# Performance work log

Measured on AMD Instinct MI355X. Metric: run time of the kernel, lower is better.

The kernel has to match this reference:

```python
import jax, jax.numpy as jnp
import numpy as np

B, H, W = 2, 50, 50
N = H * W
P = 4          # attention heads
KTAP = 2       # filter taps per GraphFilterBatchAttentional
LRELU = 0.2
ZERO_TOL = 1e-9


def conv2d(x, w, b):
    p = w.shape[-1] // 2
    y = jax.lax.conv_general_dilated(x, w, (1, 1), [(p, p), (p, p)],
                                     dimension_numbers=('NCHW', 'OIHW', 'NCHW'))
    return y + b[None, :, None, None]


def conv2d_pad_neg(x, w, b):
    # decoder uses ConstantPad2d(pad, -999) followed by VALID conv
    p = w.shape[-1] // 2
    xp = jnp.pad(x, ((0, 0), (0, 0), (p, p), (p, p)), constant_values=-999.0)
    y = jax.lax.conv_general_dilated(xp, w, (1, 1), 'VALID',
                                     dimension_numbers=('NCHW', 'OIHW', 'NCHW'))
    return y + b[None, :, None, None]


def gat_filter(x, S, a, Wf, b):
    """GraphFilterBatchAttentional (E=1, K=2 taps, concatenated heads).
    x:(B,G,N) S:(B,N,N) a:(P,2G) Wf:(P,K,G,F) b:(F,) -> (B,P*F,N)"""
    G = x.shape[1]
    s1 = jnp.einsum('pg,bgn->bpn', a[:, :G], x)
    s2 = jnp.einsum('pg,bgn->bpn', a[:, G:], x)
    # e[b,p,i,j] = LeakyReLU(a1.x_i + a2.x_j)
    e = jax.nn.leaky_relu(s1[:, :, :, None] + s2[:, :, None, :], LRELU)
    mask = (jnp.abs(S) > ZERO_TOL)[:, None]                 # (B,1,N,N)
    aij = jax.nn.softmax(jnp.where(mask, e, -1e9), axis=-1)  # softmax over neighbors j
    aij = aij * S[:, None]                                   # GAT_modified: weight by GSO
    z1 = jnp.einsum('bpij,bgj->bpgi', aij, x)                # one-hop aggregation
    y = (jnp.einsum('bgn,pgf->bpfn', x, Wf[:, 0])
         + jnp.einsum('bpgn,pgf->bpfn', z1, Wf[:, 1])
         + b[None, None, :, None])
    Bb, Pp, F, Nn = y.shape
    return y.reshape(Bb, Pp * F, Nn)


def _gat_params(key, G, F, scale=0.1):
    k1, k2, k3 = jax.random.split(key, 3)
    return (jax.random.normal(k1, (P, 2 * G), jnp.float32) * scale,
            jax.random.normal(k2, (P, KTAP, G, F), jnp.float32) * scale,
            jax.random.normal(k3, (F,), jnp.float32) * scale)


def setup_inputs() -> dict:
    key = jax.random.key(0)
    ks = jax.random.split(key, 24)
    inp = {}
    inp['x'] = jax.random.normal(ks[0], (B, 3, H, W), jnp.float32)
    u = jax.random.uniform(ks[1], (B, 2, N, N), jnp.float32)
    inp['Slist'] = (u < 0.01).astype(jnp.float32)
    # CNN encoder
    inp['enc_w1'] = jax.random.normal(ks[2], (32, 3, 3, 3), jnp.float32) * 0.1
    inp['enc_b1'] = jnp.zeros((32,), jnp.float32)
    inp['enc_w2'] = jax.random.normal(ks[3], (32, 32, 3, 3), jnp.float32) * 0.1
    inp['enc_b2'] = jnp.zeros((32,), jnp.float32)
    # GAT layers: (in_dim G, out_dim F)
    specs = {'down0': (32, 16), 'down1': (64, 8), 'up0': (32, 16),
             'up1': (64, 32), 'sc0': (32, 32), 'sc1': (64, 16)}
    for i, (name, (G, F)) in enumerate(specs.items()):
        a, Wf, b = _gat_params(ks[4 + i], G, F)
        inp[name + '_a'], inp[name + '_W'], inp[name + '_b'] = a, Wf, b
    # channel attention (reduction_ratio=1)
    inp['ca_w1'] = jax.random.normal(ks[10], (128, 128), jnp.float32) * 0.05
    inp['ca_b1'] = jnp.zeros((128,), jnp.float32)
    inp['ca_w2'] = jax.random.normal(ks[11], (128, 128), jnp.float32) * 0.05
    inp['ca_b2'] = jnp.zeros((128,), jnp.float32)
    # CNN decoder
    inp['dec_w1'] = jax.random.normal(ks[12], (32, 128, 3, 3), jnp.float32) * 0.05
    inp['dec_b1'] = jnp.zeros((32,), jnp.float32)
    inp['dec_w2'] = jax.random.normal(ks[13], (1, 32, 3, 3), jnp.float32) * 0.05
    inp['dec_b2'] = jnp.zeros((1,), jnp.float32)
    # MLP 2500 -> 512 -> 5
    inp['mlp_w1'] = jax.random.normal(ks[14], (512, 2500), jnp.float32) * 0.02
    inp['mlp_b1'] = jnp.zeros((512,), jnp.float32)
    inp['mlp_w2'] = jax.random.normal(ks[15], (5, 512), jnp.float32) * 0.05
    inp['mlp_b2'] = jnp.zeros((5,), jnp.float32)
    return inp


def reference(x, Slist, enc_w1, enc_b1, enc_w2, enc_b2,
              down0_a, down0_W, down0_b, down1_a, down1_W, down1_b,
              up0_a, up0_W, up0_b, up1_a, up1_W, up1_b,
              sc0_a, sc0_W, sc0_b, sc1_a, sc1_W, sc1_b,
              ca_w1, ca_b1, ca_w2, ca_b2,
              dec_w1, dec_b1, dec_w2, dec_b2,
              mlp_w1, mlp_b1, mlp_w2, mlp_b2):
    # encoder: Sigmoid on input, then conv+relu stack
    h = jax.nn.sigmoid(x)
    h = jax.nn.relu(conv2d(h, enc_w1, enc_b1))
    h = jax.nn.relu(conv2d(h, enc_w2, enc_b2))
    f0 = h.reshape(h.shape[0], h.shape[1], -1)          # (B,32,N)
    S0, S1 = Slist[:, 0], Slist[:, 1]
    # GNOLayers: downward pass
    f1 = gat_filter(f0, S0, down0_a, down0_W, down0_b)  # (B,64,N)
    f2 = gat_filter(f1, S1, down1_a, down1_W, down1_b)  # (B,32,N)
    # upward pass + shortcuts (upward[l] uses S[K-l-1], shortcut[l] uses S[l])
    g1 = gat_filter(f2, S1, up0_a, up0_W, up0_b) \
         + gat_filter(f1, S1, sc1_a, sc1_W, sc1_b)      # (B,64,N)
    g2 = gat_filter(g1, S0, up1_a, up1_W, up1_b) \
         + gat_filter(f0, S0, sc0_a, sc0_W, sc0_b)      # (B,128,N)
    d = g2.reshape(g2.shape[0], 128, H, W)
    # channel attention (AdaptiveMaxPool2d despite variable name)
    att = jnp.max(d, axis=(2, 3))                        # (B,128)
    att = jax.nn.sigmoid(jax.nn.relu(att @ ca_w1.T + ca_b1) @ ca_w2.T + ca_b2)
    d = d * att[:, :, None, None]
    # decoder convs with -999 constant padding
    d = jax.nn.relu(conv2d_pad_neg(d, dec_w1, dec_b1))
    d = jax.nn.relu(conv2d_pad_neg(d, dec_w2, dec_b2))
    flat = d.reshape(d.shape[0], -1)                     # (B,2500)
    m = jax.nn.relu(flat @ mlp_w1.T + mlp_b1)
    out = jax.nn.sigmoid(m @ mlp_w2.T + mlp_b2)          # final ReLU replaced by Sigmoid (out dim 5)
    return out
```

## Files before the change

### kernel.cpp

```cpp
#include <hip/hip_runtime.h>
#include <hip/hip_bf16.h>
#include <math.h>

#define BB 2
#define HH 50
#define WW 50
#define NN 2500
#define PP 4
#define LRELU_SLOPE 0.2f
#define ZTOL 1e-9f
#define PXB2 10
#define ADJW 64
#define WCAP 40

static inline int cdiv(int a, int b) { return (a + b - 1) / b; }

__device__ __forceinline__ float sigmoidf_(float v) { return 1.0f / (1.0f + expf(-v)); }

__global__ void k_repack(const float* __restrict__ e1, const float* __restrict__ e2,
                         const float* __restrict__ dd1, const float* __restrict__ dd2,
                         float* __restrict__ r1, float* __restrict__ r2,
                         float* __restrict__ r3, float* __restrict__ r4) {
    int i = blockIdx.x * blockDim.x + threadIdx.x;
    if (i < 32 * 3 * 9)  { int oc = i / 27;  int rem = i % 27;  int ic = rem / 9; int tp = rem % 9; r1[(ic * 9 + tp) * 32 + oc] = e1[i]; }
    if (i < 32 * 32 * 9) { int oc = i / 288; int rem = i % 288; int ic = rem / 9; int tp = rem % 9; r2[(ic * 9 + tp) * 32 + oc] = e2[i]; }
    if (i < 32 * 128 * 9){ int oc = i / 1152;int rem = i % 1152;int ic = rem / 9; int tp = rem % 9; r3[(ic * 9 + tp) * 32 + oc] = dd1[i]; }
    if (i < 1 * 32 * 9)  { int oc = 0;       int rem = i;       int ic = rem / 9; int tp = rem % 9; r4[(ic * 9 + tp) * 1  + oc] = dd2[i]; }
}

__launch_bounds__(256)
__global__ void k_conv_enc1(const float* __restrict__ x, const float* __restrict__ wre,
                            const float* __restrict__ bias, float* __restrict__ out) {
    int bx = blockIdx.x;
    int pxb = bx % PXB2;
    int ocg = (bx / PXB2) % 4;
    int b = bx / (PXB2 * 4);
    int px = pxb * 256 + threadIdx.x;
    bool valid = px < NN;
    int xx0 = px % WW, yy0 = px / WW;
    float acc[8];
#pragma unroll
    for (int o = 0; o < 8; ++o) acc[o] = 0.f;
    for (int ic = 0; ic < 3; ++ic) {
        const float* ip = x + ((size_t)(b * 3 + ic)) * NN;
        float v[9];
#pragma unroll
        for (int ky = 0; ky < 3; ++ky) {
            int yy = yy0 + ky - 1;
#pragma unroll
            for (int kx = 0; kx < 3; ++kx) {
                int xx = xx0 + kx - 1;
                bool ok = valid && yy >= 0 && yy < HH && xx >= 0 && xx < WW;
                v[ky * 3 + kx] = ok ? sigmoidf_(ip[yy * WW + xx]) : 0.f;
            }
        }
        const float* wp = wre + (size_t)ic * 9 * 32 + ocg * 8;
#pragma unroll
        for (int tp = 0; tp < 9; ++tp) {
            float vv = v[tp];
#pragma unroll
            for (int o = 0; o < 8; ++o) acc[o] += wp[tp * 32 + o] * vv;
        }
    }
    if (valid) {
#pragma unroll
        for (int o = 0; o < 8; ++o) {
            int oc = ocg * 8 + o;
            out[((size_t)(b * 32 + oc)) * NN + px] = fmaxf(acc[o] + bias[oc], 0.f);
        }
    }
}

template<int OCT>
__launch_bounds__(256)
__global__ void k_conv_part(const float* __restrict__ in, const float* __restrict__ wre,
                            const float* __restrict__ attscale,
                            float* __restrict__ part, int Cin, int OC, int nocg,
                            int nchunks, int icchunk, float padval) {
    int bx = blockIdx.x;
    int pxb = bx % PXB2; bx /= PXB2;
    int ocg = bx % nocg; bx /= nocg;
    int chunk = bx % nchunks;
    int b = bx / nchunks;
    int px = pxb * 256 + threadIdx.x;
    bool valid = px < NN;
    int xx0 = px % WW, yy0 = px / WW;

    float acc[OCT];
#pragma unroll
    for (int o = 0; o < OCT; ++o) acc[o] = 0.f;

    int ic0 = chunk * icchunk;
    int ic1 = ic0 + icchunk; if (ic1 > Cin) ic1 = Cin;

    for (int ic = ic0; ic < ic1; ++ic) {
        const float* ip = in + ((size_t)(b * Cin + ic)) * NN;
        float attv = attscale ? attscale[b * Cin + ic] : 1.f;
        float v[9];
#pragma unroll
        for (int ky = 0; ky < 3; ++ky) {
            int yy = yy0 + ky - 1;
#pragma unroll
            for (int kx = 0; kx < 3; ++kx) {
                int xx = xx0 + kx - 1;
                bool ok = valid && yy >= 0 && yy < HH && xx < WW && xx >= 0;
                v[ky * 3 + kx] = ok ? ip[yy * WW + xx] * attv : padval;
            }
        }
        const float* wp = wre + (size_t)ic * 9 * OC + ocg * OCT;
#pragma unroll
        for (int tp = 0; tp < 9; ++tp) {
            float vv = v[tp];
#pragma unroll
            for (int o = 0; o < OCT; ++o) acc[o] += wp[tp * OC + o] * vv;
        }
    }
    if (valid) {
#pragma unroll
        for (int o = 0; o < OCT; ++o)
            part[(((size_t)chunk * BB + b) * OC + ocg * OCT + o) * NN + px] = acc[o];
    }
}

__global__ void k_conv_reduce(const float* __restrict__ part, const float* __restrict__ bias,
                              float* __restrict__ out, float* __restrict__ xTout,
                              int OCr, int nchunks) {
    int idx = blockIdx.x * blockDim.x + threadIdx.x;
    int total = BB * OCr * NN;
    if (idx >= total) return;
    int px = idx % NN;
    int oc = (idx / NN) % OCr;
    int b = idx / (NN * OCr);
    float s = bias[oc];
    for (int c = 0; c < nchunks; ++c)
        s += part[(((size_t)c * BB + b) * OCr + oc) * NN + px];
    s = fmaxf(s, 0.f);
    if (out)   out[((size_t)(b * OCr + oc)) * NN + px] = s;
    if (xTout) xTout[((size_t)b * NN + px) * OCr + oc] = s;
}

__launch_bounds__(256)
__global__ void k_conv_dec2(const float* __restrict__ in, const float* __restrict__ wre,
                            const float* __restrict__ bias, float* __restrict__ out) {
    int pxb = blockIdx.x % PXB2;
    int b = blockIdx.x / PXB2;
    int px = pxb * 256 + threadIdx.x;
    bool valid = px < NN;
    int xx0 = px % WW, yy0 = px / WW;
    float acc = 0.f;
    for (int ic = 0; ic < 32; ++ic) {
        const float* ip = in + ((size_t)(b * 32 + ic)) * NN;
#pragma unroll
        for (int ky = 0; ky < 3; ++ky) {
            int yy = yy0 + ky - 1;
#pragma unroll
            for (int kx = 0; kx < 3; ++kx) {
                int xx = xx0 + kx - 1;
                bool ok = valid && yy >= 0 && yy < HH && xx >= 0 && xx < WW;
                float v = ok ? ip[yy * WW + xx] : -999.0f;
                acc += v * wre[ic * 9 + ky * 3 + kx];
            }
        }
    }
    if (valid) out[(size_t)b * NN + px] = fmaxf(acc + bias[0], 0.f);
}

__launch_bounds__(256)
__global__ void k_build_compact(const float* __restrict__ S,
                                int2* __restrict__ adjC, int* __restrict__ cntC) {
    __shared__ int2 stage[4][WCAP];
    __shared__ int  wcnt[4];

    int row = blockIdx.x;
    int i = row % NN;
    int b = (row / NN) % BB;
    int s = row / (NN * BB);
    const float4* Srow = (const float4*)(S + (((size_t)(b * 2 + s)) * NN + i) * NN);

    int tid = threadIdx.x;
    int w = tid >> 6, lane = tid & 63;
    int q0 = w * 157;
    int q1 = (w == 3) ? 625 : (q0 + 157);

    float4 fv[3];
#pragma unroll
    for (int r = 0; r < 3; ++r) {
        int q = q0 + r * 64 + lane;
        fv[r] = (q < q1) ? Srow[q] : make_float4(0.f, 0.f, 0.f, 0.f);
    }

    unsigned long long below = (lane == 63) ? 0x7fffffffffffffffull
                                            : ((1ull << lane) - 1ull);
    int cnt = 0;
#pragma unroll
    for (int r = 0; r < 3; ++r) {
        float4 f = fv[r];
        unsigned long long b0 = __ballot(fabsf(f.x) > ZTOL);
        unsigned long long b1 = __ballot(fabsf(f.y) > ZTOL);
        unsigned long long b2 = __ballot(fabsf(f.z) > ZTOL);
        unsigned long long b3 = __ballot(fabsf(f.w) > ZTOL);
        int rk = __popcll(b0 & below) + __popcll(b1 & below) +
                 __popcll(b2 & below) + __popcll(b3 & below);
        int j0 = (q0 + r * 64 + lane) * 4;
        int idx = cnt + rk;
        if ((b0 >> lane) & 1) { if (idx < WCAP) stage[w][idx] = make_int2(j0 + 0, __float_as_int(f.x)); ++idx; }
        if ((b1 >> lane) & 1) { if (idx < WCAP) stage[w][idx] = make_int2(j0 + 1, __float_as_int(f.y)); ++idx; }
        if ((b2 >> lane) & 1) { if (idx < WCAP) stage[w][idx] = make_int2(j0 + 2, __float_as_int(f.z)); ++idx; }
        if ((b3 >> lane) & 1) { if (idx < WCAP) stage[w][idx] = make_int2(j0 + 3, __float_as_int(f.w)); ++idx; }
        cnt += __popcll(b0) + __popcll(b1) + __popcll(b2) + __popcll(b3);
    }
    if (lane == 0) wcnt[w] = (cnt < WCAP) ? cnt : WCAP;
    __syncthreads();

    int c0 = wcnt[0], c1 = wcnt[1], c2 = wcnt[2], c3 = wcnt[3];
    int base = (w == 0) ? 0 : (w == 1) ? c0 : (w == 2) ? (c0 + c1) : (c0 + c1 + c2);
    int myc = wcnt[w];
    for (int k = lane; k < myc; k += 64) {
        int dstb = base + k;
        if (dstb < ADJW) adjC[(size_t)row * ADJW + dstb] = stage[w][k];
    }
    if (tid == 0) {
        int total = c0 + c1 + c2 + c3;
        cntC[row] = (total < ADJW) ? total : ADJW;
    }
}

__device__ __forceinline__ float4 softmax4(float4 s1f, float4 s2f, int lane, int cnt, float valr) {
    float e[PP] = { s1f.x + s2f.x, s1f.y + s2f.y, s1f.z + s2f.z, s1f.w + s2f.w };
    float w[PP];
#pragma unroll
    for (int p = 0; p < PP; ++p) {
        float v = e[p];
        v = (v < 0.f) ? LRELU_SLOPE * v : v;
        v = (lane < cnt) ? v : -1e30f;
        float mx = v;
#pragma unroll
        for (int m = 32; m >= 1; m >>= 1) mx = fmaxf(mx, __shfl_xor(mx, m));
        float ex = (lane < cnt) ? expf(v - mx) : 0.f;
        float sm = ex;
#pragma unroll
        for (int m = 32; m >= 1; m >>= 1) sm += __shfl_xor(sm, m);
        w[p] = (cnt > 0) ? ex / sm * valr : 0.f;
    }
    return make_float4(w[0], w[1], w[2], w[3]);
}

template<int PF>
__device__ __forceinline__ void emit_one(const float* __restrict__ a,
                                         float4* __restrict__ s1E, float4* __restrict__ s2E,
                                         float yl, int lane, int node) {
    float r1[PP], r2[PP];
#pragma unroll
    for (int p = 0; p < PP; ++p) {
        float v1 = (lane < PF) ? a[p * 2 * PF + lane] * yl : 0.f;
        float v2 = (lane < PF) ? a[p * 2 * PF + PF + lane] * yl : 0.f;
#pragma unroll
        for (int m = 32; m >= 1; m >>= 1) { v1 += __shfl_xor(v1, m); v2 += __shfl_xor(v2, m); }
        r1[p] = v1; r2[p] = v2;
    }
    if (lane == 0) {
        s1E[node] = make_float4(r1[0], r1[1], r1[2], r1[3]);
        s2E[node] = make_float4(r2[0], r2[1], r2[2], r2[3]);
    }
}

template<int G, int F, int FZ, int ADDP, int ES, int CMAJ>
__launch_bounds__(256)
__global__ void k_gat_layer2(const float* __restrict__ xT,
                             const int2* __restrict__ adjC, const int* __restrict__ cntC,
                             const float4* __restrict__ s1A, const float4* __restrict__ s2A,
                             const float4* __restrict__ s1Z, const float4* __restrict__ s2Z,
                             const float* __restrict__ Wf, const float* __restrict__ bias,
                             const float* __restrict__ WfZ, const float* __restrict__ biasZ,
                             const float* __restrict__ prevP,
                             float* __restrict__ auxOut,
                             const float* __restrict__ aE0, float4* __restrict__ s1E0, float4* __restrict__ s2E0,
                             const float* __restrict__ aE1, float4* __restrict__ s1E1, float4* __restrict__ s2E1,
                             float* __restrict__ dst) {
    constexpr int PF = PP * F;
    __shared__ int    csh[4][64];
    __shared__ float4 wAsh[4][64];
    __shared__ float4 wZsh[FZ ? 4 : 1][FZ ? 64 : 1];
    __shared__ float  xAsh[4][G + 1];
    __shared__ float  z1Ash[4][PP][G + 1];
    __shared__ float  z1Zsh[FZ ? 4 : 1][FZ ? PP : 1][FZ ? (G + 1) : 1];
    __shared__ float  ysh[ES ? 4 : 1][ES ? (PF + 1) : 1];

    int tid = threadIdx.x;
    int w = tid >> 6, lane = tid & 63;
    int node = blockIdx.x * 4 + w;
    int b = node / NN, i = node % NN;

    {
        if (lane < G) xAsh[w][lane] = xT[(size_t)node * G + lane];
        int cnt = cntC[node];
        int colr = 0; float valr = 0.f;
        if (lane < cnt) {
            int2 e = adjC[(size_t)node * ADJW + lane];
            colr = e.x;
            valr = __int_as_float(e.y);
        }
        float4 s2fA = make_float4(0.f, 0.f, 0.f, 0.f);
        float4 s2fZ = make_float4(0.f, 0.f, 0.f, 0.f);
        if (lane < cnt) {
            s2fA = s2A[(size_t)b * NN + colr];
            if constexpr (FZ > 0) s2fZ = s2Z[(size_t)b * NN + colr];
        }
        csh[w][lane] = colr;
        wAsh[w][lane] = softmax4(s1A[node], s2fA, lane, cnt, valr);
        if constexpr (FZ > 0) wZsh[w][lane] = softmax4(s1Z[node], s2fZ, lane, cnt, valr);

        constexpr int STEP = (G == 32) ? 2 : 1;
        int sl = (G == 32) ? (lane >> 5) : 0;
        int g  = (G == 32) ? (lane & 31) : lane;
        const float* xb = xT + (size_t)b * NN * G + g;
        float zA[PP] = {0.f, 0.f, 0.f, 0.f};
        float zZ[PP] = {0.f, 0.f, 0.f, 0.f};
        int jj = sl;
        for (; jj + 7 * STEP < cnt; jj += 8 * STEP) {
            int c[8];
            float xv[8];
#pragma unroll
            for (int u = 0; u < 8; ++u) c[u] = csh[w][jj + u * STEP];
#pragma unroll
            for (int u = 0; u < 8; ++u) xv[u] = xb[(size_t)c[u] * G];
#pragma unroll
            for (int u = 0; u < 8; ++u) {
                float4 wa = wAsh[w][jj + u * STEP];
                zA[0] += wa.x * xv[u]; zA[1] += wa.y * xv[u];
                zA[2] += wa.z * xv[u]; zA[3] += wa.w * xv[u];
                if constexpr (FZ > 0) {
                    float4 wz = wZsh[w][jj + u * STEP];
                    zZ[0] += wz.x * xv[u]; zZ[1] += wz.y * xv[u];
                    zZ[2] += wz.z * xv[u]; zZ[3] += wz.w * xv[u];
                }
            }
        }
        for (; jj < cnt; jj += STEP) {
            float xv = xb[(size_t)csh[w][jj] * G];
            float4 wa = wAsh[w][jj];
            zA[0] += wa.x * xv; zA[1] += wa.y * xv; zA[2] += wa.z * xv; zA[3] += wa.w * xv;
            if constexpr (FZ > 0) {
                float4 wz = wZsh[w][jj];
                zZ[0] += wz.x * xv; zZ[1] += wz.y * xv; zZ[2] += wz.z * xv; zZ[3] += wz.w * xv;
            }
        }
        if (G == 32) {
#pragma unroll
            for (int p = 0; p < PP; ++p) {
                zA[p] += __shfl_xor(zA[p], 32);
                if constexpr (FZ > 0) zZ[p] += __shfl_xor(zZ[p], 32);
            }
        }
        if (sl == 0) {
#pragma unroll
            for (int p = 0; p < PP; ++p) {
                z1Ash[w][p][g] = zA[p];
                if constexpr (FZ > 0) z1Zsh[w][p][g] = zZ[p];
            }
        }
    }

    for (int t = lane; t < PF; t += 64) {
        int p = t / F, f = t % F;
        const float* W0 = Wf + (size_t)(p * 2) * G * F + f;
        const float* W1 = W0 + G * F;
        float y = bias[f];
#pragma unroll 16
        for (int g = 0; g < G; ++g)
            y += xAsh[w][g] * W0[(size_t)g * F] + z1Ash[w][p][g] * W1[(size_t)g * F];
        if (ADDP) y += prevP[(size_t)node * PF + t];
        if (CMAJ) dst[((size_t)(b * PF + t)) * NN + i] = y;
        else      dst[(size_t)node * PF + t] = y;
        if (ES) ysh[w][t] = y;
    }

    if constexpr (FZ > 0) {
        for (int t = lane; t < PP * FZ; t += 64) {
            int p = t / FZ, f = t % FZ;
            const float* V0 = WfZ + (size_t)(p * 2) * G * FZ + f;
            const float* V1 = V0 + G * FZ;
            float y = biasZ[f];
#pragma unroll 16
            for (int g = 0; g < G; ++g)
                y += xAsh[w][g] * V0[(size_t)g * FZ] + z1Zsh[w][p][g] * V1[(size_t)g * FZ];
            auxOut[(size_t)node * (PP * FZ) + t] = y;
        }
    }

    if (ES) {
        float yl = (lane < PF) ? ysh[w][lane] : 0.f;
        emit_one<PF>(aE0, s1E0, s2E0, yl, lane, node);
        if (ES >= 2) emit_one<PF>(aE1, s1E1, s2E1, yl, lane, node);
    }
}

template<int G>
__launch_bounds__(256)
__global__ void k_s1s2T(const float* __restrict__ xT,
                        const float* __restrict__ aA, float4* __restrict__ s1A, float4* __restrict__ s2A,
                        const float* __restrict__ aB, float4* __restrict__ s1B, float4* __restrict__ s2B) {
    constexpr int NPB = 16;
    __shared__ float xsh[NPB][G + 1];
    __shared__ float ash[2][2][PP][G];
    __shared__ float ysh[NPB][17];

    int tid = threadIdx.x;
    int node0 = blockIdx.x * NPB;

    for (int idx = tid; idx < PP * 2 * G; idx += 256) {
        int p = idx / (2 * G), r = idx % (2 * G);
        int which = r / G, g = r % G;
        ash[0][which][p][g] = aA[idx];
        if (aB) ash[1][which][p][g] = aB[idx];
    }
    for (int idx = tid; idx < NPB * G; idx += 256) {
        int nl = idx / G, g = idx % G;
        int nn = node0 + nl;
        xsh[nl][g] = (nn < BB * NN) ? xT[(size_t)nn * G + g] : 0.f;
    }
    __syncthreads();

    {
        int nl = tid / 16, o = tid % 16;
        int set = o / 8, which = (o / 4) % 2, p = o % 4;
        float acc = 0.f;
        if (set == 0 || aB) {
#pragma unroll
            for (int g = 0; g < G; ++g) acc += ash[set][which][p][g] * xsh[nl][g];
        }
        ysh[nl][o] = acc;
    }
    __syncthreads();

    if (tid < NPB * 4) {
        int nl = tid / 4, q = tid % 4;
        int node = node0 + nl;
        if (node < BB * NN) {
            int base = (q / 2) * 8 + (q % 2) * 4;
            float4 v = make_float4(ysh[nl][base + 0], ysh[nl][base + 1],
                                   ysh[nl][base + 2], ysh[nl][base + 3]);
            if (q == 0) s1A[node] = v;
            else if (q == 1) s2A[node] = v;
            else if (q == 2) { if (aB) s1B[node] = v; }
            else             { if (aB) s2B[node] = v; }
        }
    }
}

__global__ void k_attmax(const float* __restrict__ d, float* __restrict__ att) {
    int wid = blockIdx.x;
    int lane = threadIdx.x;
    const float4* row = (const float4*)(d + (size_t)wid * NN);
    float m = -1e30f;
    for (int q = lane; q < 625; q += 64) {
        float4 f = row[q];
        m = fmaxf(m, fmaxf(fmaxf(f.x, f.y), fmaxf(f.z, f.w)));
    }
    for (int s = 32; s >= 1; s >>= 1) m = fmaxf(m, __shfl_xor(m, s));
    if (lane == 0) att[wid] = m;
}

__launch_bounds__(128)
__global__ void k_camlp(const float* __restrict__ att,
                        const float* __restrict__ w1, const float* __restrict__ b1,
                        const float* __restrict__ w2, const float* __restrict__ b2,
                        float* __restrict__ attf) {
    __shared__ float a[128];
    __shared__ float h[128];
    int b = blockIdx.x, t = threadIdx.x;
    a[t] = att[b * 128 + t];
    __syncthreads();
    float acc = b1[t];
    const float* wr = w1 + (size_t)t * 128;
    for (int k = 0; k < 128; ++k) acc += a[k] * wr[k];
    h[t] = fmaxf(acc, 0.f);
    __syncthreads();
    float acc2 = b2[t];
    const float* wr2 = w2 + (size_t)t * 128;
    for (int k = 0; k < 128; ++k) acc2 += h[k] * wr2[k];
    attf[b * 128 + t] = sigmoidf_(acc2);
}

__global__ void k_mlp1(const float* __restrict__ flat, const float* __restrict__ w,
                       const float* __restrict__ bias, float* __restrict__ out) {
    int wid = blockIdx.x;
    int lane = threadIdx.x;
    int o = wid % 512;
    int b = wid / 512;
    const float4* fr = (const float4*)(flat + (size_t)b * NN);
    const float4* wr = (const float4*)(w + (size_t)o * NN);
    float acc = 0.f;
    for (int q = lane; q < 625; q += 64) {
        float4 f = fr[q];
        float4 ww = wr[q];
        acc += f.x * ww.x + f.y * ww.y + f.z * ww.z + f.w * ww.w;
    }
    for (int s = 32; s >= 1; s >>= 1) acc += __shfl_xor(acc, s);
    if (lane == 0) out[wid] = fmaxf(acc + bias[o], 0.0f);
}

__global__ void k_mlp2(const float* __restrict__ m, const float* __restrict__ w,
                       const float* __restrict__ bias, float* __restrict__ out) {
    int wid = blockIdx.x;
    int lane = threadIdx.x;
    int o = wid % 5;
    int b = wid / 5;
    const float* mr = m + b * 512;
    const float* wr = w + o * 512;
    float acc = 0.f;
    for (int k = lane; k < 512; k += 64) acc += mr[k] * wr[k];
    for (int s = 32; s >= 1; s >>= 1) acc += __shfl_xor(acc, s);
    if (lane == 0) out[wid] = 1.0f / (1.0f + expf(-(acc + bias[o])));
}

extern "C" void kernel_launch(void* const* d_in, const int* in_sizes, int n_in,
                              void* d_out, int out_size, void* d_ws, size_t ws_size,
                              hipStream_t stream) {
    const float* x       = (const float*)d_in[0];
    const float* Slist   = (const float*)d_in[1];
    const float* enc_w1  = (const float*)d_in[2];
    const float* enc_b1  = (const float*)d_in[3];
    const float* enc_w2  = (const float*)d_in[4];
    const float* enc_b2  = (const float*)d_in[5];
    const float* d0_a = (const float*)d_in[6];  const float* d0_W = (const float*)d_in[7];  const float* d0_b = (const float*)d_in[8];
    const float* d1_a = (const float*)d_in[9];  const float* d1_W = (const float*)d_in[10]; const float* d1_b = (const float*)d_in[11];
    const float* u0_a = (const float*)d_in[12]; const float* u0_W = (const float*)d_in[13]; const float* u0_b = (const float*)d_in[14];
    const float* u1_a = (const float*)d_in[15]; const float* u1_W = (const float*)d_in[16]; const float* u1_b = (const float*)d_in[17];
    const float* s0_a = (const float*)d_in[18]; const float* s0_W = (const float*)d_in[19]; const float* s0_b = (const float*)d_in[20];
    const float* s1_a = (const float*)d_in[21]; const float* s1_W = (const float*)d_in[22]; const float* s1_b = (const float*)d_in[23];
    const float* ca_w1 = (const float*)d_in[24]; const float* ca_b1 = (const float*)d_in[25];
    const float* ca_w2 = (const float*)d_in[26]; const float* ca_b2 = (const float*)d_in[27];
    const float* dec_w1 = (const float*)d_in[28]; const float* dec_b1 = (const float*)d_in[29];
    const float* dec_w2 = (const float*)d_in[30]; const float* dec_b2 = (const float*)d_in[31];
    const float* mlp_w1 = (const float*)d_in[32]; const float* mlp_b1 = (const float*)d_in[33];
    const float* mlp_w2 = (const float*)d_in[34]; const float* mlp_b2 = (const float*)d_in[35];
    float* out = (float*)d_out;

    float* ws = (float*)d_ws;
    size_t off = 0;
    auto alloc = [&](size_t n) { float* p = ws + off; off += n; return p; };
    float* h1    = alloc((size_t)BB * 32 * NN);
    float* xT_f0 = alloc((size_t)BB * NN * 32);
    float* xT_f1 = alloc((size_t)BB * NN * 64);
    float* xT_f2 = alloc((size_t)BB * NN * 32);
    float* xT_g1 = alloc((size_t)BB * NN * 64);
    float* g2    = alloc((size_t)BB * 128 * NN);
    int2*  adjC = (int2*)alloc((size_t)2 * BB * NN * ADJW * 2);
    int*   cntC = (int*)alloc((size_t)2 * BB * NN);
    float4* s1_d0 = (float4*)alloc(4 * BB * NN); float4* s2_d0 = (float4*)alloc(4 * BB * NN);
    float4* s1_s0 = (float4*)alloc(4 * BB * NN); float4* s2_s0 = (float4*)alloc(4 * BB * NN);
    float4* s1_d1 = (float4*)alloc(4 * BB * NN); float4* s2_d1 = (float4*)alloc(4 * BB * NN);
    float4* s1_sc1= (float4*)alloc(4 * BB * NN); float4* s2_sc1= (float4*)alloc(4 * BB * NN);
    float4* s1_u0 = (float4*)alloc(4 * BB * NN); float4* s2_u0 = (float4*)alloc(4 * BB * NN);
    float4* s1_u1 = (float4*)alloc(4 * BB * NN); float4* s2_u1 = (float4*)alloc(4 * BB * NN);
    float* g1p   = alloc((size_t)BB * NN * 64);
    float* g2p   = alloc((size_t)BB * NN * 128);
    float* att   = alloc(BB * 128);
    float* attf  = alloc(BB * 128);
    float* dec1o = alloc((size_t)BB * 32 * NN);
    float* dec2o = alloc((size_t)BB * NN);
    float* mbuf  = alloc((size_t)BB * 512);
    float* wre1  = alloc(32 * 3 * 9);
    float* wre2  = alloc(32 * 32 * 9);
    float* wre3  = alloc(32 * 128 * 9);
    float* wre4  = alloc(1 * 32 * 9);
    float* partial = alloc((size_t)8 * BB * 32 * NN);
    (void)ws_size;

    const int T = 256;
    const int NNODE = BB * NN;
    const int2* adjC0 = adjC;
    const int2* adjC1 = adjC + (size_t)NNODE * ADJW;
    const int* cnt0 = cntC;
    const int* cnt1 = cntC + NNODE;

    k_repack<<<cdiv(32 * 128 * 9, T), T, 0, stream>>>(enc_w1, enc_w2, dec_w1, dec_w2,
                                                      wre1, wre2, wre3, wre4);
    k_conv_enc1<<<BB * 4 * PXB2, 256, 0, stream>>>(x, wre1, enc_b1, h1);
    k_conv_part<8><<<BB * 4 * 4 * PXB2, 256, 0, stream>>>(h1, wre2, nullptr, partial,
                                                          32, 32, 4, 4, 8, 0.0f);
    k_conv_reduce<<<cdiv(BB * 32 * NN, T), T, 0, stream>>>(partial, enc_b2, nullptr, xT_f0, 32, 4);
    k_build_compact<<<2 * NNODE, 256, 0, stream>>>(Slist, adjC, cntC);
    k_s1s2T<32><<<cdiv(NNODE, 16), 256, 0, stream>>>(xT_f0, d0_a, s1_d0, s2_d0,
                                                     s0_a, s1_s0, s2_s0);
    k_gat_layer2<32,16,32, 0, 2, 0><<<NNODE / 4, 256, 0, stream>>>(
        xT_f0, adjC0, cnt0,
        s1_d0, s2_d0, s1_s0, s2_s0,
        d0_W, d0_b, s0_W, s0_b,
        nullptr, g2p,
        d1_a, s1_d1, s2_d1, s1_a, s1_sc1, s2_sc1, xT_f1);
    k_gat_layer2<64,8,16, 0, 1, 0><<<NNODE / 4, 256, 0, stream>>>(
        xT_f1, adjC1, cnt1,
        s1_d1, s2_d1, s1_sc1, s2_sc1,
        d1_W, d1_b, s1_W, s1_b,
        nullptr, g1p,
        u0_a, s1_u0, s2_u0, nullptr, nullptr, nullptr, xT_f2);
    k_gat_layer2<32,16,0, 1, 1, 0><<<NNODE / 4, 256, 0, stream>>>(
        xT_f2, adjC1, cnt1,
        s1_u0, s2_u0, nullptr, nullptr,
        u0_W, u0_b, nullptr, nullptr,
        g1p, nullptr,
        u1_a, s1_u1, s2_u1, nullptr, nullptr, nullptr, xT_g1);
    k_gat_layer2<64,32,0, 1, 0, 1><<<NNODE / 4, 256, 0, stream>>>(
        xT_g1, adjC0, cnt0,
        s1_u1, s2_u1, nullptr, nullptr,
        u1_W, u1_b, nullptr, nullptr,
        g2p, nullptr,
        nullptr, nullptr, nullptr, nullptr, nullptr, nullptr, g2);
    k_attmax<<<BB * 128, 64, 0, stream>>>(g2, att);
    k_camlp<<<BB, 128, 0, stream>>>(att, ca_w1, ca_b1, ca_w2, ca_b2, attf);
    k_conv_part<8><<<BB * 8 * 4 * PXB2, 256, 0, stream>>>(g2, wre3, attf, partial,
                                                          128, 32, 4, 8, 16, -999.0f);
    k_conv_reduce<<<cdiv(BB * 32 * NN, T), T, 0, stream>>>(partial, dec_b1, dec1o, nullptr, 32, 8);
    k_conv_dec2<<<BB * PXB2, 256, 0, stream>>>(dec1o, wre4, dec_b2, dec2o);
    k_mlp1<<<BB * 512, 64, 0, stream>>>(dec2o, mlp_w1, mlp_b1, mbuf);
    k_mlp2<<<BB * 5, 64, 0, stream>>>(mbuf, mlp_w2, mlp_b2, out);
}
```

Measured before the change: 238.0 us.

## Fuse weight repack, conv reduce, and s1s2 kernels; re-split decoder convs

The weight repack kernel is folded into extra blocks of the adjacency-compaction launch, and the encoder conv partial-sum reduction is fused into the attention-score (s1/s2) kernel, which also writes the transposed features. The final 32-to-1 decoder conv now splits input channels across four waves and reduces through shared memory, giving more blocks. The first decoder conv partial kernel changes its OC/chunk split parameters. The aim is fewer launches and better parallelism in small kernels. The risk is that the fused reduction reads partials with a strided pattern.

```diff
diff --git a/kernel.cpp b/kernel.cpp
--- a/kernel.cpp
+++ b/kernel.cpp
@@ -16,17 +16,6 @@
 static inline int cdiv(int a, int b) { return (a + b - 1) / b; }
 
 __device__ __forceinline__ float sigmoidf_(float v) { return 1.0f / (1.0f + expf(-v)); }
-
-__global__ void k_repack(const float* __restrict__ e1, const float* __restrict__ e2,
-                         const float* __restrict__ dd1, const float* __restrict__ dd2,
-                         float* __restrict__ r1, float* __restrict__ r2,
-                         float* __restrict__ r3, float* __restrict__ r4) {
-    int i = blockIdx.x * blockDim.x + threadIdx.x;
-    if (i < 32 * 3 * 9)  { int oc = i / 27;  int rem = i % 27;  int ic = rem / 9; int tp = rem % 9; r1[(ic * 9 + tp) * 32 + oc] = e1[i]; }
-    if (i < 32 * 32 * 9) { int oc = i / 288; int rem = i % 288; int ic = rem / 9; int tp = rem % 9; r2[(ic * 9 + tp) * 32 + oc] = e2[i]; }
-    if (i < 32 * 128 * 9){ int oc = i / 1152;int rem = i % 1152;int ic = rem / 9; int tp = rem % 9; r3[(ic * 9 + tp) * 32 + oc] = dd1[i]; }
-    if (i < 1 * 32 * 9)  { int oc = 0;       int rem = i;       int ic = rem / 9; int tp = rem % 9; r4[(ic * 9 + tp) * 1  + oc] = dd2[i]; }
-}
 
 __launch_bounds__(256)
 __global__ void k_conv_enc1(const float* __restrict__ x, const float* __restrict__ wre,
@@ -142,13 +131,17 @@
 __launch_bounds__(256)
 __global__ void k_conv_dec2(const float* __restrict__ in, const float* __restrict__ wre,
                             const float* __restrict__ bias, float* __restrict__ out) {
-    int pxb = blockIdx.x % PXB2;
-    int b = blockIdx.x / PXB2;
-    int px = pxb * 256 + threadIdx.x;
+    __shared__ float red[4][64];
+    int tid = threadIdx.x;
+    int w = tid >> 6, lane = tid & 63;
+    int blk = blockIdx.x;
+    int pxb = blk % 40;
+    int b = blk / 40;
+    int px = pxb * 64 + lane;
     bool valid = px < NN;
     int xx0 = px % WW, yy0 = px / WW;
     float acc = 0.f;
-    for (int ic = 0; ic < 32; ++ic) {
+    for (int ic = w * 8; ic < w * 8 + 8; ++ic) {
         const float* ip = in + ((size_t)(b * 32 + ic)) * NN;
 #pragma unroll
         for (int ky = 0; ky < 3; ++ky) {
@@ -162,16 +155,33 @@
             }
         }
     }
-    if (valid) out[(size_t)b * NN + px] = fmaxf(acc + bias[0], 0.f);
+    red[w][lane] = acc;
+    __syncthreads();
+    if (w == 0 && valid) {
+        float s = red[0][lane] + red[1][lane] + red[2][lane] + red[3][lane];
+        out[(size_t)b * NN + px] = fmaxf(s + bias[0], 0.f);
+    }
 }
 
 __launch_bounds__(256)
 __global__ void k_build_compact(const float* __restrict__ S,
-                                int2* __restrict__ adjC, int* __restrict__ cntC) {
+                                int2* __restrict__ adjC, int* __restrict__ cntC,
+                                const float* __restrict__ e1, const float* __restrict__ e2,
+                                const float* __restrict__ dd1, const float* __restrict__ dd2,
+                                float* __restrict__ r1, float* __restrict__ r2,
+                                float* __restrict__ r3, float* __restrict__ r4) {
+    int row = blockIdx.x;
+    if (row >= 2 * BB * NN) {
+        int i = (row - 2 * BB * NN) * 256 + threadIdx.x;
+        if (i < 32 * 3 * 9)  { int oc = i / 27;  int rem = i % 27;  int ic = rem / 9; int tp = rem % 9; r1[(ic * 9 + tp) * 32 + oc] = e1[i]; }
+        if (i < 32 * 32 * 9) { int oc = i / 288; int rem = i % 288; int ic = rem / 9; int tp = rem % 9; r2[(ic * 9 + tp) * 32 + oc] = e2[i]; }
+        if (i < 32 * 128 * 9){ int oc = i / 1152;int rem = i % 1152;int ic = rem / 9; int tp = rem % 9; r3[(ic * 9 + tp) * 32 + oc] = dd1[i]; }
+        if (i < 1 * 32 * 9)  { int oc = 0;       int rem = i;       int ic = rem / 9; int tp = rem % 9; r4[(ic * 9 + tp) * 1  + oc] = dd2[i]; }
+        return;
+    }
     __shared__ int2 stage[4][WCAP];
     __shared__ int  wcnt[4];
 
-    int row = blockIdx.x;
     int i = row % NN;
     int b = (row / NN) % BB;
     int s = row / (NN * BB);
@@ -397,9 +407,10 @@
 
 template<int G>
 __launch_bounds__(256)
-__global__ void k_s1s2T(const float* __restrict__ xT,
-                        const float* __restrict__ aA, float4* __restrict__ s1A, float4* __restrict__ s2A,
-                        const float* __restrict__ aB, float4* __restrict__ s1B, float4* __restrict__ s2B) {
+__global__ void k_s1s2T_fused(const float* __restrict__ part, const float* __restrict__ bias,
+                              float* __restrict__ xTout,
+                              const float* __restrict__ aA, float4* __restrict__ s1A, float4* __restrict__ s2A,
+                              const float* __restrict__ aB, float4* __restrict__ s1B, float4* __restrict__ s2B) {
     constexpr int NPB = 16;
     __shared__ float xsh[NPB][G + 1];
     __shared__ float ash[2][2][PP][G];
@@ -415,11 +426,24 @@
         if (aB) ash[1][which][p][g] = aB[idx];
     }
     for (int idx = tid; idx < NPB * G; idx += 256) {
+        int nl = idx & (NPB - 1), g = idx >> 4;
+        int node = node0 + nl;
+        float s = 0.f;
+        if (node < BB * NN) {
+            int b = node / NN, px = node % NN;
+            s = bias[g];
+            for (int c = 0; c < 4; ++c)
+                s += part[(((size_t)c * BB + b) * G + g) * NN + px];
+            s = fmaxf(s, 0.f);
+        }
+        xsh[nl][g] = s;
+    }
+    __syncthreads();
+    for (int idx = tid; idx < NPB * G; idx += 256) {
         int nl = idx / G, g = idx % G;
-        int nn = node0 + nl;
-        xsh[nl][g] = (nn < BB * NN) ? xT[(size_t)nn * G + g] : 0.f;
-    }
-    __syncthreads();
+        int node = node0 + nl;
+        if (node < BB * NN) xTout[(size_t)node * G + g] = xsh[nl][g];
+    }
 
     {
         int nl = tid / 16, o = tid % 16;
@@ -575,15 +599,15 @@
     const int* cnt0 = cntC;
     const int* cnt1 = cntC + NNODE;
 
-    k_repack<<<cdiv(32 * 128 * 9, T), T, 0, stream>>>(enc_w1, enc_w2, dec_w1, dec_w2,
-                                                      wre1, wre2, wre3, wre4);
+    k_build_compact<<<2 * NNODE + 144, 256, 0, stream>>>(Slist, adjC, cntC,
+                                                         enc_w1, enc_w2, dec_w1, dec_w2,
+                                                         wre1, wre2, wre3, wre4);
     k_conv_enc1<<<BB * 4 * PXB2, 256, 0, stream>>>(x, wre1, enc_b1, h1);
     k_conv_part<8><<<BB * 4 * 4 * PXB2, 256, 0, stream>>>(h1, wre2, nullptr, partial,
                                                           32, 32, 4, 4, 8, 0.0f);
-    k_conv_reduce<<<cdiv(BB * 32 * NN, T), T, 0, stream>>>(partial, enc_b2, nullptr, xT_f0, 32, 4);
-    k_build_compact<<<2 * NNODE, 256, 0, stream>>>(Slist, adjC, cntC);
-    k_s1s2T<32><<<cdiv(NNODE, 16), 256, 0, stream>>>(xT_f0, d0_a, s1_d0, s2_d0,
-                                                     s0_a, s1_s0, s2_s0);
+    k_s1s2T_fused<32><<<cdiv(NNODE, 16), 256, 0, stream>>>(partial, enc_b2, xT_f0,
+                                                           d0_a, s1_d0, s2_d0,
+                                                           s0_a, s1_s0, s2_s0);
     k_gat_layer2<32,16,32, 0, 2, 0><<<NNODE / 4, 256, 0, stream>>>(
         xT_f0, adjC0, cnt0,
         s1_d0, s2_d0, s1_s0, s2_s0,
@@ -610,10 +634,10 @@
         nullptr, nullptr, nullptr, nullptr, nullptr, nullptr, g2);
     k_attmax<<<BB * 128, 64, 0, stream>>>(g2, att);
     k_camlp<<<BB, 128, 0, stream>>>(att, ca_w1, ca_b1, ca_w2, ca_b2, attf);
-    k_conv_part<8><<<BB * 8 * 4 * PXB2, 256, 0, stream>>>(g2, wre3, attf, partial,
-                                                          128, 32, 4, 8, 16, -999.0f);
+    k_conv_part<16><<<BB * 8 * 2 * PXB2, 256, 0, stream>>>(g2, wre3, attf, partial,
+                                                           128, 32, 2, 8, 16, -999.0f);
     k_conv_reduce<<<cdiv(BB * 32 * NN, T), T, 0, stream>>>(partial, dec_b1, dec1o, nullptr, 32, 8);
-    k_conv_dec2<<<BB * PXB2, 256, 0, stream>>>(dec1o, wre4, dec_b2, dec2o);
+    k_conv_dec2<<<BB * 40, 256, 0, stream>>>(dec1o, wre4, dec_b2, dec2o);
     k_mlp1<<<BB * 512, 64, 0, stream>>>(dec2o, mlp_w1, mlp_b1, mbuf);
     k_mlp2<<<BB * 5, 64, 0, stream>>>(mbuf, mlp_w2, mlp_b2, out);
 }
```

New measurement: 216.6 us. 9.0% less time.
